# Performance work log

Hardware: AMD Instinct MI355X
Metric: run time of the kernel (lower is better)

## Reference

```python
import jax, jax.numpy as jnp
import numpy as np

B, L, V, E, H2, M, OOV = 128, 400, 50000, 512, 1024, 1024, 50


def setup_inputs() -> dict:
    key = jax.random.key(0)
    ks = jax.random.split(key, 14)
    s = 0.02
    return {
        "y": jax.random.randint(ks[0], (B,), 0, V),
        "h": jax.random.normal(ks[1], (1, B, H2), jnp.float32),
        "memory_bank": jax.random.normal(ks[2], (B, L, M), jnp.float32),
        "src_mask": jnp.ones((B, L), jnp.float32),
        "max_num_oovs": OOV,
        "src_oov": jax.random.randint(ks[3], (B, L), 0, V + OOV),
        # learned parameters (PyTorch Linear y = x @ W + b with W stored [in, out])
        "emb": jax.random.normal(ks[4], (V, E), jnp.float32) * s,
        "W_ih": jax.random.normal(ks[5], (E, 3 * H2), jnp.float32) * s,   # GRU input weights (r|z|n)
        "W_hh": jax.random.normal(ks[6], (H2, 3 * H2), jnp.float32) * s,  # GRU hidden weights (r|z|n)
        "b_ih": jnp.zeros((3 * H2,), jnp.float32),
        "b_hh": jnp.zeros((3 * H2,), jnp.float32),
        "W_mem": jax.random.normal(ks[7], (M, H2), jnp.float32) * s,      # attention memory_project (no bias)
        "W_dec": jax.random.normal(ks[8], (H2, H2), jnp.float32) * s,     # attention decode_project
        "b_dec": jnp.zeros((H2,), jnp.float32),
        "v": jax.random.normal(ks[9], (H2,), jnp.float32) * s,            # attention score vector (no bias)
        "W_pgen": jax.random.normal(ks[10], (M + H2 + E, 1), jnp.float32) * s,
        "b_pgen": jnp.zeros((1,), jnp.float32),
        "W_v1": jax.random.normal(ks[11], (M + H2, H2), jnp.float32) * s,
        "b_v1": jnp.zeros((H2,), jnp.float32),
        "W_v2": jax.random.normal(ks[12], (H2, V), jnp.float32) * s,
        "b_v2": jnp.zeros((V,), jnp.float32),
    }


def reference(y, h, memory_bank, src_mask, max_num_oovs, src_oov,
              emb, W_ih, W_hh, b_ih, b_hh, W_mem, W_dec, b_dec, v,
              W_pgen, b_pgen, W_v1, b_v1, W_v2, b_v2):
    # --- embedding lookup (single decode step) ---
    y_emb = emb[y]                                    # [B, E]
    h0 = h[-1]                                        # [B, H2]

    # --- one-step GRU (PyTorch gate order r, z, n); dropout is identity (eval) ---
    gi = y_emb @ W_ih + b_ih                          # [B, 3*H2]
    gh = h0 @ W_hh + b_hh
    i_r, i_z, i_n = jnp.split(gi, 3, axis=-1)
    h_r, h_z, h_n = jnp.split(gh, 3, axis=-1)
    r = jax.nn.sigmoid(i_r + h_r)
    z = jax.nn.sigmoid(i_z + h_z)
    n = jnp.tanh(i_n + r * h_n)
    h_next = (1.0 - z) * n + z * h0                   # [B, H2]

    # --- concat (Bahdanau) attention with masked softmax ---
    enc_feat = jnp.einsum('blm,mh->blh', memory_bank, W_mem)   # [B, L, H2]
    dec_feat = h_next @ W_dec + b_dec                           # [B, H2]
    scores = jnp.tanh(enc_feat + dec_feat[:, None, :]) @ v     # [B, L]
    attn = jax.nn.softmax(scores, axis=1) * src_mask
    attn_dist = attn / attn.sum(axis=1, keepdims=True)         # renormalized masked softmax
    context = jnp.einsum('bl,blm->bm', attn_dist, memory_bank) # [B, M]

    # --- vocab distribution ---
    vd_in = jnp.concatenate([context, h_next], axis=1)          # [B, M+H2]
    logits = (vd_in @ W_v1 + b_v1) @ W_v2 + b_v2                # [B, V]
    vocab_dist = jax.nn.softmax(logits, axis=1)

    # --- generation gate ---
    pg_in = jnp.concatenate([context, h_next, y_emb], axis=1)   # [B, M+H2+E]
    p_gen = jax.nn.sigmoid(pg_in @ W_pgen + b_pgen)             # [B, 1]

    # --- copy mechanism: scatter attention mass into extended vocab ---
    vocab_dist_ = p_gen * vocab_dist
    attn_dist_ = (1.0 - p_gen) * attn_dist
    bsz = vocab_dist_.shape[0]
    if max_num_oovs > 0:
        vocab_dist_ = jnp.concatenate(
            [vocab_dist_, jnp.zeros((bsz, max_num_oovs), vocab_dist_.dtype)], axis=1)
    rows = jnp.arange(bsz)[:, None]
    final_dist = vocab_dist_.at[rows, src_oov].add(attn_dist_)  # [B, V+OOV]

    return final_dist, h_next[None], context, attn_dist, p_gen
```

## Files before the change

kernel.cpp:

```cpp
#include <hip/hip_runtime.h>

#define B_   128
#define L_   400
#define V_   50000
#define E_   512
#define H2_  1024
#define M_   1024
#define OOV_ 50
#define VE_  50050
#define BL_  51200

typedef __attribute__((ext_vector_type(8))) short short8;
typedef __attribute__((ext_vector_type(4))) float f32x4;

__device__ __forceinline__ unsigned short f2bf(float f){
  unsigned int u = __builtin_bit_cast(unsigned int, f);
  u = (u + 0x7FFFu + ((u >> 16) & 1u)) >> 16;
  return (unsigned short)u;
}
__device__ __forceinline__ float bf2f(unsigned short s){
  unsigned int u = ((unsigned int)s) << 16;
  return __builtin_bit_cast(float, u);
}

__device__ __forceinline__ void gl_lds16(const void* g, void* l){
  __builtin_amdgcn_global_load_lds(
      (const __attribute__((address_space(1))) unsigned int*)g,
      (__attribute__((address_space(3))) unsigned int*)l, 16, 0, 0);
}

__device__ __forceinline__ float wredsum(float v){
  #pragma unroll
  for (int o = 32; o > 0; o >>= 1) v += __shfl_xor(v, o);
  return v;
}
__device__ __forceinline__ float wredmax(float v){
  #pragma unroll
  for (int o = 32; o > 0; o >>= 1) v = fmaxf(v, __shfl_xor(v, o));
  return v;
}

__global__ void phase1_kernel(const float* __restrict__ mb, unsigned char* __restrict__ mbT,
                              const float* __restrict__ Wm, unsigned char* __restrict__ WTt,
                              const int* __restrict__ y, const float* __restrict__ emb,
                              float* __restrict__ yemb, float* __restrict__ zeroA,
                              float* __restrict__ ctx)
{
  __shared__ float tile[32][33];
  int bid = blockIdx.x, t = threadIdx.x;
  if (bid < 25600){
    int u = bid * 256 + t;
    int gr  = u >> 7;
    int m16 = u & 127;
    const float* src = mb + (size_t)gr * 1024 + m16 * 8;
    float4 f0 = *(const float4*)src;
    float4 f1 = *(const float4*)(src + 4);
    uint4 w;
    w.x = (unsigned)f2bf(f0.x) | ((unsigned)f2bf(f0.y) << 16);
    w.y = (unsigned)f2bf(f0.z) | ((unsigned)f2bf(f0.w) << 16);
    w.z = (unsigned)f2bf(f1.x) | ((unsigned)f2bf(f1.y) << 16);
    w.w = (unsigned)f2bf(f1.z) | ((unsigned)f2bf(f1.w) << 16);
    int panel = gr >> 7, r = gr & 127;
    int ks = m16 >> 3, c16 = m16 & 7;
    size_t dst = (size_t)panel * 262144 + (size_t)ks * 16384
               + (size_t)((r * 128 + c16 * 16) ^ ((r & 7) << 4));
    *(uint4*)(mbT + dst) = w;
  } else if (bid < 26624){
    int b2 = bid - 25600;
    int n0 = (b2 & 31) * 32, k0 = (b2 >> 5) * 32;
    int tx = t & 31, ty = t >> 5;
    #pragma unroll
    for (int i = 0; i < 32; i += 8) tile[ty + i][tx] = Wm[(size_t)(k0 + ty + i) * H2_ + n0 + tx];
    __syncthreads();
    if (t < 128){
      int nn = t & 31, k16 = t >> 5;
      int col = n0 + nn, kb = k0 + k16 * 8;
      uint4 w;
      w.x = (unsigned)f2bf(tile[k16*8+0][nn]) | ((unsigned)f2bf(tile[k16*8+1][nn]) << 16);
      w.y = (unsigned)f2bf(tile[k16*8+2][nn]) | ((unsigned)f2bf(tile[k16*8+3][nn]) << 16);
      w.z = (unsigned)f2bf(tile[k16*8+4][nn]) | ((unsigned)f2bf(tile[k16*8+5][nn]) << 16);
      w.w = (unsigned)f2bf(tile[k16*8+6][nn]) | ((unsigned)f2bf(tile[k16*8+7][nn]) << 16);
      int cpn = col >> 7, r = col & 127;
      int ks = kb >> 6, c16 = (kb & 63) >> 3;
      size_t dst = (size_t)cpn * 262144 + (size_t)ks * 16384
                 + (size_t)((r * 128 + c16 * 16) ^ ((r & 7) << 4));
      *(uint4*)(WTt + dst) = w;
    }
  } else if (bid < 26688){
    int idx = (bid - 26624) * 256 + t;
    int b  = idx >> 7;
    int c4 = (idx & 127) << 2;
    float4 v = *(const float4*)(emb + (size_t)y[b] * E_ + c4);
    *(float4*)(yemb + (size_t)b * E_ + c4) = v;
  } else if (bid < 27762){
    int u = (bid - 26688) * 256 + t;
    float4 z = {0.f, 0.f, 0.f, 0.f};
    *(float4*)(zeroA + (size_t)u * 4) = z;
  } else {
    int u = (bid - 27762) * 256 + t;
    float4 z = {0.f, 0.f, 0.f, 0.f};
    *(float4*)(ctx + (size_t)u * 4) = z;
  }
}

__device__ __forceinline__ void gemm128_body(int bx, int by,
                               const float* __restrict__ A, int lda,
                               const float* __restrict__ W, int ldw,
                               const float* __restrict__ bias,
                               float* __restrict__ C, int ldc,
                               int N, int kChunk, int addBias)
{
  int tid = threadIdx.x;
  int wv = tid >> 6, lane = tid & 63, lr = lane & 15, lhi = lane >> 4;
  int colBase = bx * 128 + wv * 32;
  int colL[2];
  colL[0] = min(colBase + lr, N - 1);
  colL[1] = min(colBase + 16 + lr, N - 1);
  int k0 = by * kChunk;

  f32x4 zero = {0.f, 0.f, 0.f, 0.f};
  f32x4 acc[8][2];
  #pragma unroll
  for (int r = 0; r < 8; r++){ acc[r][0] = zero; acc[r][1] = zero; }

  int nks = kChunk >> 5;
  for (int ks = 0; ks < nks; ++ks){
    int k = k0 + ks * 32 + lhi * 8;
    short8 bf[2];
    #pragma unroll
    for (int cf = 0; cf < 2; cf++){
      #pragma unroll
      for (int j = 0; j < 8; j++)
        bf[cf][j] = (short)f2bf(W[(size_t)(k + j) * ldw + colL[cf]]);
    }
    #pragma unroll
    for (int rf = 0; rf < 8; rf++){
      const float* ap = A + (size_t)(rf * 16 + lr) * lda + k;
      float4 a0 = *(const float4*)ap;
      float4 a1 = *(const float4*)(ap + 4);
      short8 af;
      af[0]=(short)f2bf(a0.x); af[1]=(short)f2bf(a0.y); af[2]=(short)f2bf(a0.z); af[3]=(short)f2bf(a0.w);
      af[4]=(short)f2bf(a1.x); af[5]=(short)f2bf(a1.y); af[6]=(short)f2bf(a1.z); af[7]=(short)f2bf(a1.w);
      acc[rf][0] = __builtin_amdgcn_mfma_f32_16x16x32_bf16(af, bf[0], acc[rf][0], 0, 0, 0);
      acc[rf][1] = __builtin_amdgcn_mfma_f32_16x16x32_bf16(af, bf[1], acc[rf][1], 0, 0, 0);
    }
  }

  bool addB = addBias && (by == 0);
  #pragma unroll
  for (int cf = 0; cf < 2; cf++){
    int col = colBase + cf * 16 + lr;
    bool ok = col < N;
    float bv = addB ? bias[colL[cf]] : 0.f;
    #pragma unroll
    for (int rf = 0; rf < 8; rf++)
      #pragma unroll
      for (int i = 0; i < 4; i++){
        int row = rf * 16 + lhi * 4 + i;
        if (ok) atomicAdd(&C[(size_t)row * ldc + col], acc[rf][cf][i] + bv);
      }
  }
}

__launch_bounds__(256)
__global__ void gemm128_kernel(const float* __restrict__ A, int lda,
                               const float* __restrict__ W, int ldw,
                               const float* __restrict__ bias,
                               float* __restrict__ C, int ldc,
                               int N, int kChunk, int addBias){
  gemm128_body(blockIdx.x, blockIdx.y, A, lda, W, ldw, bias, C, ldc, N, kChunk, addBias);
}

__launch_bounds__(256)
__global__ void gigh_kernel(const float* __restrict__ yemb, const float* __restrict__ hin,
                            const float* __restrict__ W_ih, const float* __restrict__ W_hh,
                            float* __restrict__ gi, float* __restrict__ gh){
  int bid = blockIdx.x;
  if (bid < 48)
    gemm128_body(bid % 24, bid / 24, yemb, E_,  W_ih, 3 * H2_, nullptr, gi, 3 * H2_, 3 * H2_, 256, 0);
  else {
    int b2 = bid - 48;
    gemm128_body(b2 % 24, b2 / 24, hin, H2_, W_hh, 3 * H2_, nullptr, gh, 3 * H2_, 3 * H2_, 256, 0);
  }
}

__launch_bounds__(256)
__global__ void gemm_v1_kernel(const float* __restrict__ A1, const float* __restrict__ A2,
                               const float* __restrict__ W,
                               const float* __restrict__ bias,
                               float* __restrict__ C, int N, int kChunk)
{
  int tid = threadIdx.x;
  int wv = tid >> 6, lane = tid & 63, lr = lane & 15, lhi = lane >> 4;
  int colBase = blockIdx.x * 128 + wv * 32;
  int halfY = gridDim.y >> 1;
  const float* Asrc = (blockIdx.y < halfY) ? A1 : A2;
  int yk = (blockIdx.y < halfY) ? blockIdx.y : (blockIdx.y - halfY);
  int k0 = yk * kChunk;
  int wk0 = blockIdx.y * kChunk;

  f32x4 zero = {0.f, 0.f, 0.f, 0.f};
  f32x4 acc[8][2];
  #pragma unroll
  for (int r = 0; r < 8; r++){ acc[r][0] = zero; acc[r][1] = zero; }

  int nks = kChunk >> 5;
  for (int ks = 0; ks < nks; ++ks){
    int k  = k0 + ks * 32 + lhi * 8;
    int wk = wk0 + ks * 32 + lhi * 8;
    short8 bf[2];
    #pragma unroll
    for (int cf = 0; cf < 2; cf++){
      #pragma unroll
      for (int j = 0; j < 8; j++)
        bf[cf][j] = (short)f2bf(W[(size_t)(wk + j) * H2_ + colBase + cf * 16 + lr]);
    }
    #pragma unroll
    for (int rf = 0; rf < 8; rf++){
      const float* ap = Asrc + (size_t)(rf * 16 + lr) * 1024 + k;
      float4 a0 = *(const float4*)ap;
      float4 a1 = *(const float4*)(ap + 4);
      short8 af;
      af[0]=(short)f2bf(a0.x); af[1]=(short)f2bf(a0.y); af[2]=(short)f2bf(a0.z); af[3]=(short)f2bf(a0.w);
      af[4]=(short)f2bf(a1.x); af[5]=(short)f2bf(a1.y); af[6]=(short)f2bf(a1.z); af[7]=(short)f2bf(a1.w);
      acc[rf][0] = __builtin_amdgcn_mfma_f32_16x16x32_bf16(af, bf[0], acc[rf][0], 0, 0, 0);
      acc[rf][1] = __builtin_amdgcn_mfma_f32_16x16x32_bf16(af, bf[1], acc[rf][1], 0, 0, 0);
    }
  }

  bool addB = (blockIdx.y == 0);
  #pragma unroll
  for (int cf = 0; cf < 2; cf++){
    int col = colBase + cf * 16 + lr;
    float bv = addB ? bias[col] : 0.f;
    #pragma unroll
    for (int rf = 0; rf < 8; rf++)
      #pragma unroll
      for (int i = 0; i < 4; i++){
        int row = rf * 16 + lhi * 4 + i;
        atomicAdd(&C[(size_t)row * H2_ + col], acc[rf][cf][i] + bv);
      }
  }
}

__launch_bounds__(256)
__global__ void gemm_bfA_kernel(const unsigned short* __restrict__ A,
                                const float* __restrict__ W,
                                const float* __restrict__ bias,
                                float* __restrict__ C0, float* __restrict__ C1,
                                int N, int kChunk)
{
  int tid = threadIdx.x;
  int wv = tid >> 6, lane = tid & 63, lr = lane & 15, lhi = lane >> 4;
  int colBase = blockIdx.x * 128 + wv * 32;
  int colL[2];
  colL[0] = min(colBase + lr, N - 1);
  colL[1] = min(colBase + 16 + lr, N - 1);
  int k0 = blockIdx.y * kChunk;
  float* Cw = (blockIdx.y == 0) ? C0 : C1;

  f32x4 zero = {0.f, 0.f, 0.f, 0.f};
  f32x4 acc[8][2];
  #pragma unroll
  for (int r = 0; r < 8; r++){ acc[r][0] = zero; acc[r][1] = zero; }

  int nks = kChunk >> 5;
  for (int ks = 0; ks < nks; ++ks){
    int k = k0 + ks * 32 + lhi * 8;
    short8 bf[2];
    #pragma unroll
    for (int cf = 0; cf < 2; cf++){
      #pragma unroll
      for (int j = 0; j < 8; j++)
        bf[cf][j] = (short)f2bf(W[(size_t)(k + j) * N + colL[cf]]);
    }
    #pragma unroll
    for (int rf = 0; rf < 8; rf++){
      short8 af = *(const short8*)(A + (size_t)(rf * 16 + lr) * 1024 + k);
      acc[rf][0] = __builtin_amdgcn_mfma_f32_16x16x32_bf16(af, bf[0], acc[rf][0], 0, 0, 0);
      acc[rf][1] = __builtin_amdgcn_mfma_f32_16x16x32_bf16(af, bf[1], acc[rf][1], 0, 0, 0);
    }
  }

  bool addB = (blockIdx.y == 0);
  #pragma unroll
  for (int cf = 0; cf < 2; cf++){
    int col = colBase + cf * 16 + lr;
    bool ok = col < N;
    float bv = addB ? bias[colL[cf]] : 0.f;
    #pragma unroll
    for (int rf = 0; rf < 8; rf++)
      #pragma unroll
      for (int i = 0; i < 4; i++){
        int row = rf * 16 + lhi * 4 + i;
        if (ok) Cw[(size_t)row * V_ + col] = acc[rf][cf][i] + bv;
      }
  }
}

__global__ void gru_gates_kernel(const float* __restrict__ gi, const float* __restrict__ gh,
                                 const float* __restrict__ bih, const float* __restrict__ bhh,
                                 const float* __restrict__ h0, float* __restrict__ hn){
  int idx = blockIdx.x * 256 + threadIdx.x;
  int b = idx >> 10, j = idx & 1023;
  const float* gib = gi + (size_t)b * 3072;
  const float* ghb = gh + (size_t)b * 3072;
  float ir = gib[j]        + bih[j],        hr = ghb[j]        + bhh[j];
  float iz = gib[j + 1024] + bih[j + 1024], hz = ghb[j + 1024] + bhh[j + 1024];
  float in_= gib[j + 2048] + bih[j + 2048], hnv= ghb[j + 2048] + bhh[j + 2048];
  float r = 1.f / (1.f + __expf(-(ir + hr)));
  float z = 1.f / (1.f + __expf(-(iz + hz)));
  float n = tanhf(in_ + r * hnv);
  hn[idx] = (1.f - z) * n + z * h0[idx];
}

__launch_bounds__(512, 2)
__global__ void scores_kernel(const unsigned char* __restrict__ mbT,
                              const unsigned char* __restrict__ WTt,
                              const float* __restrict__ dec, const float* __restrict__ vvec,
                              float* __restrict__ scr)
{
  __shared__ __align__(16) unsigned char LDSm[131072];
  const int tid = threadIdx.x, lane = tid & 63;
  const int wv = tid >> 6, lr = lane & 15, lhi = lane >> 4;
  const int wru = wv >> 2, wcu = wv & 3;

  int p = blockIdx.x;
  int lid = (p & 7) * 100 + (p >> 3);
  int rp = lid >> 2, cp = lid & 3;
  int r0 = rp << 8;

  int wvu = __builtin_amdgcn_readfirstlane(wv);
  int idx4 = wvu & 3, half = idx4 >> 1, sub = idx4 & 1;
  const unsigned char* seg = (wvu < 4 ? mbT + (size_t)(2 * rp + half) * 262144
                                      : WTt + (size_t)(2 * cp + half) * 262144)
                             + sub * 8192 + lane * 16;
  const int segLds = (wvu < 4 ? 0 : 32768) + idx4 * 8192;

  int aoff[8], boff[4];
  #pragma unroll
  for (int rf = 0; rf < 8; rf++){
    int row = wru * 128 + rf * 16 + lr;
    aoff[rf] = (row * 128 + lhi * 16) ^ ((row & 7) << 4);
  }
  #pragma unroll
  for (int cf = 0; cf < 4; cf++){
    int col = wcu * 64 + cf * 16 + lr;
    boff[cf] = 32768 + ((col * 128 + lhi * 16) ^ ((col & 7) << 4));
  }

  f32x4 zero = {0.f, 0.f, 0.f, 0.f};
  f32x4 acc[8][4];
  #pragma unroll
  for (int rf = 0; rf < 8; rf++)
    #pragma unroll
    for (int cf = 0; cf < 4; cf++) acc[rf][cf] = zero;

  #pragma unroll
  for (int j = 0; j < 8; j++)
    gl_lds16(seg + j * 1024, &LDSm[segLds + j * 1024]);

  #pragma unroll 1
  for (int t = 0; t < 16; ++t){
    const int cur = (t & 1) << 16;
    if (t < 15){
      const unsigned char* s = seg + (size_t)(t + 1) * 16384;
      const int nb = ((t + 1) & 1) << 16;
      #pragma unroll
      for (int j = 0; j < 8; j++)
        gl_lds16(s + j * 1024, &LDSm[nb + segLds + j * 1024]);
      asm volatile("s_waitcnt vmcnt(8)" ::: "memory");
    } else {
      asm volatile("s_waitcnt vmcnt(0)" ::: "memory");
    }
    __builtin_amdgcn_sched_barrier(0);
    __builtin_amdgcn_s_barrier();
    __builtin_amdgcn_sched_barrier(0);
    #pragma unroll
    for (int k2 = 0; k2 < 2; k2++){
      short8 af[8], bfr[4];
      #pragma unroll
      for (int rf = 0; rf < 8; rf++) af[rf]  = *(const short8*)&LDSm[cur + (aoff[rf] ^ (k2 << 6))];
      #pragma unroll
      for (int cf = 0; cf < 4; cf++) bfr[cf] = *(const short8*)&LDSm[cur + (boff[cf] ^ (k2 << 6))];
      __builtin_amdgcn_s_setprio(1);
      #pragma unroll
      for (int rf = 0; rf < 8; rf++)
        #pragma unroll
        for (int cf = 0; cf < 4; cf++)
          acc[rf][cf] = __builtin_amdgcn_mfma_f32_16x16x32_bf16(af[rf], bfr[cf], acc[rf][cf], 0, 0, 0);
      __builtin_amdgcn_s_setprio(0);
    }
    __builtin_amdgcn_sched_barrier(0);
    asm volatile("s_waitcnt lgkmcnt(0)" ::: "memory");
    __builtin_amdgcn_s_barrier();
    __builtin_amdgcn_sched_barrier(0);
  }

  int colb = (cp << 8) + wcu * 64 + lr;
  float vv0 = vvec[colb], vv1 = vvec[colb + 16], vv2 = vvec[colb + 32], vv3 = vvec[colb + 48];
  #pragma unroll
  for (int rf = 0; rf < 8; rf++){
    #pragma unroll
    for (int i = 0; i < 4; i++){
      int grow = r0 + wru * 128 + rf * 16 + lhi * 4 + i;
      int bb = grow / 400;
      const float* dp = dec + (size_t)bb * 1024 + colb;
      float x0 = acc[rf][0][i] + dp[0];
      float x1 = acc[rf][1][i] + dp[16];
      float x2 = acc[rf][2][i] + dp[32];
      float x3 = acc[rf][3][i] + dp[48];
      float part = (1.f - 2.f / (__expf(2.f * x0) + 1.f)) * vv0
                 + (1.f - 2.f / (__expf(2.f * x1) + 1.f)) * vv1
                 + (1.f - 2.f / (__expf(2.f * x2) + 1.f)) * vv2
                 + (1.f - 2.f / (__expf(2.f * x3) + 1.f)) * vv3;
      part += __shfl_xor(part, 1);
      part += __shfl_xor(part, 2);
      part += __shfl_xor(part, 4);
      part += __shfl_xor(part, 8);
      if (lr == 0) atomicAdd(&scr[grow], part);
    }
  }
}

__global__ void attn_softmax_kernel(const float* __restrict__ scores, const float* __restrict__ mask,
                                    float* __restrict__ attn){
  int b = blockIdx.x, t = threadIdx.x;
  int wv = t >> 6, lane = t & 63;
  __shared__ float red[4];
  float s0 = (t < 400)       ? scores[b * 400 + t]       : -1e30f;
  float s1 = (t + 256 < 400) ? scores[b * 400 + t + 256] : -1e30f;
  float m = wredmax(fmaxf(s0, s1));
  if (lane == 0) red[wv] = m;
  __syncthreads();
  float M = fmaxf(fmaxf(red[0], red[1]), fmaxf(red[2], red[3]));
  __syncthreads();
  float e0 = (t < 400)       ? __expf(s0 - M) * mask[b * 400 + t]       : 0.f;
  float e1 = (t + 256 < 400) ? __expf(s1 - M) * mask[b * 400 + t + 256] : 0.f;
  float s = wredsum(e0 + e1);
  if (lane == 0) red[wv] = s;
  __syncthreads();
  float inv = 1.f / (red[0] + red[1] + red[2] + red[3]);
  if (t < 400)       attn[b * 400 + t]       = e0 * inv;
  if (t + 256 < 400) attn[b * 400 + t + 256] = e1 * inv;
}

__launch_bounds__(256)
__global__ void context_kernel(const float* __restrict__ attn, const unsigned char* __restrict__ mbT,
                               float* __restrict__ ctx){
  int b = blockIdx.y, lc = blockIdx.x, t = threadIdx.x;
  int u = t & 127;
  int half = t >> 7;
  __shared__ float a[100];
  if (t < 100) a[t] = attn[b * 400 + lc * 100 + t];
  __syncthreads();
  int ks = u >> 3, c16 = u & 7;
  float s[8];
  #pragma unroll
  for (int j = 0; j < 8; j++) s[j] = 0.f;
  for (int l = half; l < 100; l += 2){
    int gr = b * 400 + lc * 100 + l;
    int panel = gr >> 7, r = gr & 127;
    const unsigned char* pp = mbT + (size_t)panel * 262144 + (size_t)ks * 16384
                              + (size_t)((r * 128 + c16 * 16) ^ ((r & 7) << 4));
    short8 v = *(const short8*)pp;
    float al = a[l];
    #pragma unroll
    for (int j = 0; j < 8; j++) s[j] += al * bf2f((unsigned short)v[j]);
  }
  float* cp = ctx + (size_t)b * M_ + u * 8;
  #pragma unroll
  for (int j = 0; j < 8; j++) atomicAdd(cp + j, s[j]);
}

__global__ void pgen_kernel(const float* __restrict__ ctx, const float* __restrict__ hn,
                            const float* __restrict__ yemb,
                            const float* __restrict__ Wp, const float* __restrict__ bp,
                            float* __restrict__ pg){
  int b = blockIdx.x, t = threadIdx.x, wv = t >> 6, lane = t & 63;
  __shared__ float red[4];
  float s = 0.f;
  for (int i = t; i < 1024; i += 256) s += ctx[(size_t)b * 1024 + i] * Wp[i];
  for (int i = t; i < 1024; i += 256) s += hn[(size_t)b * 1024 + i] * Wp[1024 + i];
  for (int i = t; i < 512;  i += 256) s += yemb[(size_t)b * 512 + i] * Wp[2048 + i];
  s = wredsum(s);
  if (lane == 0) red[wv] = s;
  __syncthreads();
  if (t == 0){
    float S = red[0] + red[1] + red[2] + red[3] + bp[0];
    pg[b] = 1.f / (1.f + __expf(-S));
  }
}

__global__ void hid2bf_kernel(const float* __restrict__ hid, unsigned short* __restrict__ hb){
  int idx = blockIdx.x * 256 + threadIdx.x;
  float4 v = *(const float4*)(hid + (size_t)idx * 4);
  ushort2 p0 = {f2bf(v.x), f2bf(v.y)};
  ushort2 p1 = {f2bf(v.z), f2bf(v.w)};
  *(ushort2*)(hb + (size_t)idx * 4)     = p0;
  *(ushort2*)(hb + (size_t)idx * 4 + 2) = p1;
}

__global__ void vocab_softmax_kernel(float* __restrict__ lg0, const float* __restrict__ lg1,
                                     const float* __restrict__ pg,
                                     const float* __restrict__ attn, const int* __restrict__ soov,
                                     float* __restrict__ fin){
  int b = blockIdx.x, t = threadIdx.x, wv = t >> 6, lane = t & 63;
  __shared__ float redm[16], reds[16];
  float* l0 = lg0 + (size_t)b * V_;
  const float* l1 = lg1 + (size_t)b * V_;
  float m = -1e30f, s = 0.f;
  for (int i = t; i < V_; i += 1024){
    float l = l0[i] + l1[i];
    l0[i] = l;
    float mn = fmaxf(m, l);
    s = s * __expf(m - mn) + __expf(l - mn);
    m = mn;
  }
  #pragma unroll
  for (int o = 32; o > 0; o >>= 1){
    float mo = __shfl_xor(m, o), so = __shfl_xor(s, o);
    float mn = fmaxf(m, mo);
    s = s * __expf(m - mn) + so * __expf(mo - mn);
    m = mn;
  }
  if (lane == 0){ redm[wv] = m; reds[wv] = s; }
  __syncthreads();
  float M = -1e30f;
  #pragma unroll
  for (int w = 0; w < 16; w++) M = fmaxf(M, redm[w]);
  float S = 0.f;
  #pragma unroll
  for (int w = 0; w < 16; w++) S += reds[w] * __expf(redm[w] - M);
  float pgb = pg[b];
  float scale = pgb / S;
  float* fb = fin + (size_t)b * VE_;
  for (int i = t; i < V_; i += 1024) fb[i] = __expf(l0[i] - M) * scale;
  for (int i = V_ + t; i < VE_; i += 1024) fb[i] = 0.f;
  __syncthreads();
  float om = 1.f - pgb;
  if (t < 400) atomicAdd(&fb[soov[b * 400 + t]], om * attn[b * 400 + t]);
}

extern "C" void kernel_launch(void* const* d_in, const int* in_sizes, int n_in,
                              void* d_out, int out_size, void* d_ws, size_t ws_size,
                              hipStream_t stream)
{
  const int*   y     = (const int*)  d_in[0];
  const float* hin   = (const float*)d_in[1];
  const float* mb    = (const float*)d_in[2];
  const float* mask  = (const float*)d_in[3];
  const int*   soov  = (const int*)  d_in[5];
  const float* emb   = (const float*)d_in[6];
  const float* W_ih  = (const float*)d_in[7];
  const float* W_hh  = (const float*)d_in[8];
  const float* b_ih  = (const float*)d_in[9];
  const float* b_hh  = (const float*)d_in[10];
  const float* W_mem = (const float*)d_in[11];
  const float* W_dec = (const float*)d_in[12];
  const float* b_dec = (const float*)d_in[13];
  const float* vvec  = (const float*)d_in[14];
  const float* W_pg  = (const float*)d_in[15];
  const float* b_pg  = (const float*)d_in[16];
  const float* W_v1  = (const float*)d_in[17];
  const float* b_v1  = (const float*)d_in[18];
  const float* W_v2  = (const float*)d_in[19];
  const float* b_v2  = (const float*)d_in[20];

  float* out   = (float*)d_out;
  float* fin   = out;
  float* hnext = out + (size_t)B_ * VE_;
  float* ctx   = hnext + (size_t)B_ * H2_;
  float* attn  = ctx + (size_t)B_ * M_;
  float* pg    = attn + (size_t)B_ * L_;

  float* ws   = (float*)d_ws;
  float* yemb = ws;
  float* gi   = ws + 65536;
  float* gh   = gi + 393216;
  float* dec  = gh + 393216;
  float* scr  = dec + 131072;
  float* hid  = scr + 51200;
  float* lg0  = hid + 131072;
  unsigned short* hidbf = (unsigned short*)(lg0 + 6400000);
  unsigned char*  WTt   = (unsigned char*)(hidbf + 131072);
  unsigned char*  mbT   = WTt + 2097152;
  float* lg1  = (float*)mbT;

  phase1_kernel<<<27890, 256, 0, stream>>>(mb, mbT, W_mem, WTt, y, emb, yemb, gi, ctx);

  gigh_kernel<<<144, 256, 0, stream>>>(yemb, hin, W_ih, W_hh, gi, gh);
  gru_gates_kernel<<<512, 256, 0, stream>>>(gi, gh, b_ih, b_hh, hin, hnext);
  gemm128_kernel<<<dim3(8, 4), 256, 0, stream>>>(hnext, H2_, W_dec, H2_, b_dec, dec, H2_, H2_, 256, 1);

  scores_kernel<<<800, 512, 0, stream>>>(mbT, WTt, dec, vvec, scr);
  attn_softmax_kernel<<<128, 256, 0, stream>>>(scr, mask, attn);
  context_kernel<<<dim3(4, 128), 256, 0, stream>>>(attn, mbT, ctx);

  pgen_kernel<<<128, 256, 0, stream>>>(ctx, hnext, yemb, W_pg, b_pg, pg);
  gemm_v1_kernel<<<dim3(8, 8), 256, 0, stream>>>(ctx, hnext, W_v1, b_v1, hid, H2_, 256);
  hid2bf_kernel<<<128, 256, 0, stream>>>(hid, hidbf);
  gemm_bfA_kernel<<<dim3(391, 2), 256, 0, stream>>>(hidbf, W_v2, b_v2, lg0, lg1, V_, 512);

  vocab_softmax_kernel<<<128, 1024, 0, stream>>>(lg0, lg1, pg, attn, soov, fin);
}
```

Before: 577.5 us.

## Split GEMM K-step into four barrier-synced phases interleaving loads and MFMA

```diff
diff --git a/kernel.cpp b/kernel.cpp
--- a/kernel.cpp
+++ b/kernel.cpp
@@ -363,36 +363,97 @@
   #pragma unroll 1
   for (int t = 0; t < 16; ++t){
     const int cur = (t & 1) << 16;
+    const int nb  = ((t + 1) & 1) << 16;
+    const unsigned char* snext = seg + (size_t)(t + 1) * 16384;
     if (t < 15){
-      const unsigned char* s = seg + (size_t)(t + 1) * 16384;
-      const int nb = ((t + 1) & 1) << 16;
-      #pragma unroll
-      for (int j = 0; j < 8; j++)
-        gl_lds16(s + j * 1024, &LDSm[nb + segLds + j * 1024]);
-      asm volatile("s_waitcnt vmcnt(8)" ::: "memory");
+      #pragma unroll
+      for (int j = 0; j < 4; j++)
+        gl_lds16(snext + j * 1024, &LDSm[nb + segLds + j * 1024]);
+      asm volatile("s_waitcnt vmcnt(4)" ::: "memory");
     } else {
       asm volatile("s_waitcnt vmcnt(0)" ::: "memory");
     }
     __builtin_amdgcn_sched_barrier(0);
     __builtin_amdgcn_s_barrier();
     __builtin_amdgcn_sched_barrier(0);
-    #pragma unroll
-    for (int k2 = 0; k2 < 2; k2++){
-      short8 af[8], bfr[4];
-      #pragma unroll
-      for (int rf = 0; rf < 8; rf++) af[rf]  = *(const short8*)&LDSm[cur + (aoff[rf] ^ (k2 << 6))];
-      #pragma unroll
-      for (int cf = 0; cf < 4; cf++) bfr[cf] = *(const short8*)&LDSm[cur + (boff[cf] ^ (k2 << 6))];
-      __builtin_amdgcn_s_setprio(1);
-      #pragma unroll
-      for (int rf = 0; rf < 8; rf++)
-        #pragma unroll
-        for (int cf = 0; cf < 4; cf++)
-          acc[rf][cf] = __builtin_amdgcn_mfma_f32_16x16x32_bf16(af[rf], bfr[cf], acc[rf][cf], 0, 0, 0);
-      __builtin_amdgcn_s_setprio(0);
-    }
-    __builtin_amdgcn_sched_barrier(0);
+
+    short8 af[4], bfr[4];
+
+    #pragma unroll
+    for (int rf = 0; rf < 4; rf++) af[rf]  = *(const short8*)&LDSm[cur + aoff[rf]];
+    #pragma unroll
+    for (int cf = 0; cf < 4; cf++) bfr[cf] = *(const short8*)&LDSm[cur + boff[cf]];
+    __builtin_amdgcn_sched_barrier(0);
+    __builtin_amdgcn_s_barrier();
     asm volatile("s_waitcnt lgkmcnt(0)" ::: "memory");
+    __builtin_amdgcn_sched_barrier(0);
+    __builtin_amdgcn_s_setprio(1);
+    #pragma unroll
+    for (int rf = 0; rf < 4; rf++)
+      #pragma unroll
+      for (int cf = 0; cf < 4; cf++)
+        acc[rf][cf] = __builtin_amdgcn_mfma_f32_16x16x32_bf16(af[rf], bfr[cf], acc[rf][cf], 0, 0, 0);
+    __builtin_amdgcn_s_setprio(0);
+    __builtin_amdgcn_sched_barrier(0);
+    __builtin_amdgcn_s_barrier();
+    __builtin_amdgcn_sched_barrier(0);
+
+    short8 af2[4];
+    if (t < 15){
+      #pragma unroll
+      for (int j = 4; j < 8; j++)
+        gl_lds16(snext + j * 1024, &LDSm[nb + segLds + j * 1024]);
+    }
+    #pragma unroll
+    for (int rf = 0; rf < 4; rf++) af2[rf] = *(const short8*)&LDSm[cur + aoff[rf + 4]];
+    __builtin_amdgcn_sched_barrier(0);
+    __builtin_amdgcn_s_barrier();
+    asm volatile("s_waitcnt lgkmcnt(0)" ::: "memory");
+    __builtin_amdgcn_sched_barrier(0);
+    __builtin_amdgcn_s_setprio(1);
+    #pragma unroll
+    for (int rf = 0; rf < 4; rf++)
+      #pragma unroll
+      for (int cf = 0; cf < 4; cf++)
+        acc[rf + 4][cf] = __builtin_amdgcn_mfma_f32_16x16x32_bf16(af2[rf], bfr[cf], acc[rf + 4][cf], 0, 0, 0);
+    __builtin_amdgcn_s_setprio(0);
+    __builtin_amdgcn_sched_barrier(0);
+    __builtin_amdgcn_s_barrier();
+    __builtin_amdgcn_sched_barrier(0);
+
+    #pragma unroll
+    for (int rf = 0; rf < 4; rf++) af[rf]  = *(const short8*)&LDSm[cur + (aoff[rf] ^ 64)];
+    #pragma unroll
+    for (int cf = 0; cf < 4; cf++) bfr[cf] = *(const short8*)&LDSm[cur + (boff[cf] ^ 64)];
+    __builtin_amdgcn_sched_barrier(0);
+    __builtin_amdgcn_s_barrier();
+    asm volatile("s_waitcnt lgkmcnt(0)" ::: "memory");
+    __builtin_amdgcn_sched_barrier(0);
+    __builtin_amdgcn_s_setprio(1);
+    #pragma unroll
+    for (int rf = 0; rf < 4; rf++)
+      #pragma unroll
+      for (int cf = 0; cf < 4; cf++)
+        acc[rf][cf] = __builtin_amdgcn_mfma_f32_16x16x32_bf16(af[rf], bfr[cf], acc[rf][cf], 0, 0, 0);
+    __builtin_amdgcn_s_setprio(0);
+    __builtin_amdgcn_sched_barrier(0);
+    __builtin_amdgcn_s_barrier();
+    __builtin_amdgcn_sched_barrier(0);
+
+    #pragma unroll
+    for (int rf = 0; rf < 4; rf++) af2[rf] = *(const short8*)&LDSm[cur + (aoff[rf + 4] ^ 64)];
+    __builtin_amdgcn_sched_barrier(0);
+    __builtin_amdgcn_s_barrier();
+    asm volatile("s_waitcnt lgkmcnt(0)" ::: "memory");
+    __builtin_amdgcn_sched_barrier(0);
+    __builtin_amdgcn_s_setprio(1);
+    #pragma unroll
+    for (int rf = 0; rf < 4; rf++)
+      #pragma unroll
+      for (int cf = 0; cf < 4; cf++)
+        acc[rf + 4][cf] = __builtin_amdgcn_mfma_f32_16x16x32_bf16(af2[rf], bfr[cf], acc[rf + 4][cf], 0, 0, 0);
+    __builtin_amdgcn_s_setprio(0);
+    __builtin_amdgcn_sched_barrier(0);
     __builtin_amdgcn_s_barrier();
     __builtin_amdgcn_sched_barrier(0);
   }
```

Result: faster. 563.9 us (-2.3%).
